# Optimization experiments

Hardware: AMD Instinct MI355X
Metric: run time of the kernel (lower is better)

## Reference

```python
import jax, jax.numpy as jnp
import numpy as np

N = 8192      # total nodes (128 graphs x 64 electrodes)
L = 256       # signal_length
F = 64        # num_features
H = 128       # hidden_channels
G = 128       # num graphs
E = 262144    # num edges
C = 2         # n_classes


def setup_inputs() -> dict:
    key = jax.random.key(0)
    ks = jax.random.split(key, 20)
    def rn(k, shape, scale=0.05):
        return jax.random.normal(k, shape, jnp.float32) * scale
    return dict(
        x=jax.random.normal(ks[0], (N, L), jnp.float32),
        edge_index=jax.random.randint(ks[1], (2, E), 0, N),
        batch=jnp.repeat(jnp.arange(G), N // G),  # sorted graph id per node
        cw0=rn(ks[2], (F, 1, 7)), cb0=rn(ks[3], (F,)),
        cw_mid=rn(ks[4], (3, F, F, 5)), cb_mid=rn(ks[5], (3, F)),  # convs-2 = 3 middle convs
        cw_last=rn(ks[6], (F, F, 3)), cb_last=rn(ks[7], (F,)),
        enc_w=rn(ks[8], (F, F * 4)), enc_b=rn(ks[9], (F,)),  # in = F*((L-1)//2**6+1) = 256
        g0_rel_w=rn(ks[10], (H, F)), g0_rel_b=rn(ks[11], (H,)), g0_root_w=rn(ks[12], (H, F)),
        g_rel_w=rn(ks[13], (7, H, H)), g_rel_b=rn(ks[14], (7, H)), g_root_w=rn(ks[15], (7, H, H)),
        lin_w=rn(ks[16], (3, H, H)), lin_b=rn(ks[17], (3, H)),
        out_w=rn(ks[18], (C, H)), out_b=rn(ks[19], (C,)),
    )


def _conv1d(x, w, b, stride, pad):
    # x: [N, Cin, L], w: [Cout, Cin, K]
    y = jax.lax.conv_general_dilated(x, w, (stride,), [(pad, pad)],
                                     dimension_numbers=('NCH', 'OIH', 'NCH'))
    return y + b[None, :, None]


def reference(x, edge_index, batch, cw0, cb0, cw_mid, cb_mid, cw_last, cb_last,
              enc_w, enc_b, g0_rel_w, g0_rel_b, g0_root_w,
              g_rel_w, g_rel_b, g_root_w, lin_w, lin_b, out_w, out_b):
    act = jax.nn.relu
    rows = x.shape[0]
    h = x[:, None, :]                                    # [N, 1, L]
    h = act(_conv1d(h, cw0, cb0, 2, 3))                  # [N, F, L/2]
    for i in range(3):                                   # middle convs, k=5 s=2 p=2
        h = act(_conv1d(h, cw_mid[i], cb_mid[i], 2, 2))
    h = act(_conv1d(h, cw_last, cb_last, 2, 1))          # k=3 s=2 p=1 -> [N, F, 8]
    # AvgPool1d(k=3, s=2, p=1), count_include_pad=True -> always divide by 3
    h = jax.lax.reduce_window(h, 0.0, jax.lax.add, (1, 1, 3), (1, 1, 2),
                              [(0, 0), (0, 0), (1, 1)]) / 3.0   # [N, F, 4]
    h = h.reshape(rows, -1)                              # [N, F*4]
    h = h @ enc_w.T + enc_b                              # [N, F]
    src, dst = edge_index[0], edge_index[1]
    def gconv(h, rel_w, rel_b, root_w):
        # PyG GraphConv (aggr='add'): lin_rel(sum_j x_j) + lin_root(x)
        agg = jax.ops.segment_sum(h[src], dst, num_segments=N)
        return agg @ rel_w.T + rel_b + h @ root_w.T
    h = act(gconv(h, g0_rel_w, g0_rel_b, g0_root_w))     # hop 0: F -> H
    for i in range(7):                                   # hops 1..7: H -> H
        h = act(gconv(h, g_rel_w[i], g_rel_b[i], g_root_w[i]))
    # global mean pool by graph id
    sums = jax.ops.segment_sum(h, batch, num_segments=G)
    cnt = jax.ops.segment_sum(jnp.ones((N, 1), h.dtype), batch, num_segments=G)
    h = sums / jnp.maximum(cnt, 1.0)                     # [G, H]
    for i in range(3):
        h = act(h @ lin_w[i].T + lin_b[i])
    logits = h @ out_w.T + out_b                         # [G, C]
    return jax.nn.log_softmax(logits, -1)
```

## Files before the change

kernel.cpp:

```cpp
#include <hip/hip_runtime.h>
#include <hip/hip_bf16.h>

#define DEV_INLINE __device__ __forceinline__

typedef _Float16 f16;
typedef _Float16 f16x4 __attribute__((ext_vector_type(4)));
typedef _Float16 f16x8 __attribute__((ext_vector_type(8)));
typedef __bf16 bf16;
typedef __bf16 bf16x8 __attribute__((ext_vector_type(8)));
typedef float f32x16 __attribute__((ext_vector_type(16)));
typedef float f32x4 __attribute__((ext_vector_type(4)));

constexpr int N_NODES = 8192;
constexpr int G = 128;
constexpr int E_EDGES = 262144;

struct alignas(16) ConvLDS {
  union {
    char act1[2][2][66][128];
    struct {
      char act3[2][2][18][128];
      char act4[2][2][10][128];
      float act5[16][68];
      float pooled[2][256];
      float encred[2][2][64];
    } tail;
  } A;
  char act2[2][2][34][128];
  f16 xs16[2][272];
};

template<int MT, int LOG_PN, int IN_PS, int OUT_PS>
DEV_INLINE void conv_mid(const f16* __restrict__ wb, const float* __restrict__ bias,
                         char* inb, char* outb, int w, int l) {
  const int cht = w & 1;
  const int o_lane = cht * 32 + (l & 31);
  const int khalf = l >> 5;
  if ((w >> 1) < MT) {
    f16x8 wf[5][4];
#pragma unroll
    for (int k = 0; k < 5; k++)
#pragma unroll
      for (int s = 0; s < 4; s++)
        wf[k][s] = *(const f16x8*)&wb[(k * 64 + o_lane) * 64 + s * 16 + khalf * 8];
    f32x16 binit;
#pragma unroll
    for (int g = 0; g < 4; g++) {
      const float4 b4 = *(const float4*)&bias[cht * 32 + 8 * g + khalf * 4];
      binit[4 * g + 0] = b4.x; binit[4 * g + 1] = b4.y;
      binit[4 * g + 2] = b4.z; binit[4 * g + 3] = b4.w;
    }
    for (int mt = (w >> 1); mt < MT; mt += 2) {
      const int mo = mt * 32 + (l & 31);
      const int node = mo >> LOG_PN;
      const int po = mo & ((1 << LOG_PN) - 1);
      f32x16 acc = binit;
#pragma unroll
      for (int k = 0; k < 5; k++) {
        const int d = k - 2;
        const int par = d & 1;
        const int row = po + (d >> 1) + 1;
        const char* rb = inb + ((node * 2 + par) * IN_PS + row) * 128;
        const int fx = row & 7;
#pragma unroll
        for (int s = 0; s < 4; s++) {
          const int c8 = 2 * s + khalf;
          f16x8 af = *(const f16x8*)(rb + ((c8 ^ fx) << 4));
          acc = __builtin_amdgcn_mfma_f32_32x32x16_f16(wf[k][s], af, acc, 0, 0, 0);
        }
      }
      const int orow = (po >> 1) + 1;
      const int ofx = orow & 7;
      char* base = outb + ((node * 2 + (po & 1)) * OUT_PS + orow) * 128 + khalf * 8;
#pragma unroll
      for (int g = 0; g < 4; g++) {
        f16x4 h4;
        h4[0] = (f16)fmaxf(acc[4 * g + 0], 0.f);
        h4[1] = (f16)fmaxf(acc[4 * g + 1], 0.f);
        h4[2] = (f16)fmaxf(acc[4 * g + 2], 0.f);
        h4[3] = (f16)fmaxf(acc[4 * g + 3], 0.f);
        *(f16x4*)(base + (((cht * 4 + g) ^ ofx) << 4)) = h4;
      }
    }
  }
}

__global__ __launch_bounds__(256, 3) void conv_encode_kernel(
    const float* __restrict__ x,
    const f16* __restrict__ w0f, const float* __restrict__ cb0,
    const f16* __restrict__ wbmid, const float* __restrict__ cb_mid,
    const f16* __restrict__ wb5, const float* __restrict__ cb_last,
    const float* __restrict__ enc_w, const float* __restrict__ enc_b,
    float* __restrict__ henc) {
  __shared__ ConvLDS lds;
  const int tid = threadIdx.x;
  const int w = tid >> 6, l = tid & 63;
  const int n0 = blockIdx.x * 2;

  for (int idx = tid; idx < 512; idx += 256) {
    int node = idx >> 8, j = idx & 255;
    lds.xs16[node][3 + j] = (f16)x[(size_t)(n0 + node) * 256 + j];
  }
  if (tid < 64) {
    int node = tid >> 5, t = tid & 31;
    int par = (t >> 3) & 1, hi = t >> 4, j = t & 7;
    *(int4*)&lds.A.act1[node][par][hi ? 65 : 0][j * 16] = make_int4(0, 0, 0, 0);
  } else if (tid < 128) {
    int t2 = tid - 64;
    int node = t2 >> 5, t = t2 & 31;
    int par = (t >> 3) & 1, hi = t >> 4, j = t & 7;
    *(int4*)&lds.act2[node][par][hi ? 33 : 0][j * 16] = make_int4(0, 0, 0, 0);
  } else if (tid < 160) {
    int t3 = tid - 128;
    int node = t3 >> 4, s = t3 & 15;
    int slot = (s < 3) ? s : (256 + s);
    lds.xs16[node][slot] = (f16)0.f;
  }
  __syncthreads();

  {
    const int cht = w & 1;
    const int o_lane = cht * 32 + (l & 31);
    const int khalf = l >> 5;
    const f16x8 w0frag = *(const f16x8*)&w0f[o_lane * 16 + khalf * 8];
    f32x16 binit;
#pragma unroll
    for (int g = 0; g < 4; g++) {
      const float4 b4 = *(const float4*)&cb0[cht * 32 + 8 * g + khalf * 4];
      binit[4 * g + 0] = b4.x; binit[4 * g + 1] = b4.y;
      binit[4 * g + 2] = b4.z; binit[4 * g + 3] = b4.w;
    }
    for (int mt = (w >> 1); mt < 8; mt += 2) {
      const int mo = mt * 32 + (l & 31);
      const int node = mo >> 7;
      const int po = mo & 127;
      union { uint u[4]; f16x8 v; } au;
      const char* ap = (const char*)&lds.xs16[node][2 * po + khalf * 8];
#pragma unroll
      for (int j = 0; j < 4; j++) au.u[j] = *(const uint*)(ap + 4 * j);
      f32x16 acc = __builtin_amdgcn_mfma_f32_32x32x16_f16(w0frag, au.v, binit, 0, 0, 0);
      const int orow = (po >> 1) + 1;
      const int ofx = orow & 7;
      char* base = (char*)lds.A.act1 + ((node * 2 + (po & 1)) * 66 + orow) * 128 + khalf * 8;
#pragma unroll
      for (int g = 0; g < 4; g++) {
        f16x4 h4;
        h4[0] = (f16)fmaxf(acc[4 * g + 0], 0.f);
        h4[1] = (f16)fmaxf(acc[4 * g + 1], 0.f);
        h4[2] = (f16)fmaxf(acc[4 * g + 2], 0.f);
        h4[3] = (f16)fmaxf(acc[4 * g + 3], 0.f);
        *(f16x4*)(base + (((cht * 4 + g) ^ ofx) << 4)) = h4;
      }
    }
  }
  __syncthreads();

  conv_mid<4, 6, 66, 34>(wbmid, cb_mid, (char*)lds.A.act1, (char*)lds.act2, w, l);
  __syncthreads();

  if (tid < 128) {
    int which = tid >> 6;
    int t = tid & 63;
    int node = t >> 5, tt = t & 31;
    int par = (tt >> 3) & 1, hi = tt >> 4, j = tt & 7;
    if (which == 0)
      *(int4*)&lds.A.tail.act3[node][par][hi ? 17 : 0][j * 16] = make_int4(0, 0, 0, 0);
    else
      *(int4*)&lds.A.tail.act4[node][par][hi ? 9 : 0][j * 16] = make_int4(0, 0, 0, 0);
  }
  __syncthreads();

  conv_mid<2, 5, 34, 18>(wbmid + 5 * 64 * 64, cb_mid + 64,
                         (char*)lds.act2, (char*)lds.A.tail.act3, w, l);
  __syncthreads();
  conv_mid<1, 4, 18, 10>(wbmid + 2 * 5 * 64 * 64, cb_mid + 128,
                         (char*)lds.A.tail.act3, (char*)lds.A.tail.act4, w, l);
  __syncthreads();

  {
    const int ch_row = w * 16 + (l & 15);
    const int kq = l >> 4;
    f16x8 wf5[3][2];
#pragma unroll
    for (int k = 0; k < 3; k++)
#pragma unroll
      for (int s = 0; s < 2; s++)
        wf5[k][s] = *(const f16x8*)&wb5[(k * 64 + ch_row) * 64 + s * 32 + kq * 8];
    const float4 b4 = *(const float4*)&cb_last[w * 16 + kq * 4];
    f32x4 acc5 = {b4.x, b4.y, b4.z, b4.w};
    const int m5 = l & 15, nd5 = m5 >> 3, p5 = m5 & 7;
#pragma unroll
    for (int k = 0; k < 3; k++) {
      const int d = k - 1;
      const int par = d & 1;
      const int row = p5 + (d >> 1) + 1;
      const char* rb = (char*)lds.A.tail.act4 + ((nd5 * 2 + par) * 10 + row) * 128;
      const int fx = row & 7;
#pragma unroll
      for (int s = 0; s < 2; s++) {
        const int c8 = 4 * s + kq;
        f16x8 af = *(const f16x8*)(rb + ((c8 ^ fx) << 4));
        acc5 = __builtin_amdgcn_mfma_f32_16x16x32_f16(wf5[k][s], af, acc5, 0, 0, 0);
      }
    }
    f32x4 o4;
    o4[0] = fmaxf(acc5[0], 0.f);
    o4[1] = fmaxf(acc5[1], 0.f);
    o4[2] = fmaxf(acc5[2], 0.f);
    o4[3] = fmaxf(acc5[3], 0.f);
    *(f32x4*)&lds.A.tail.act5[nd5 * 8 + p5][w * 16 + kq * 4] = o4;
  }
  __syncthreads();

  for (int jj = tid; jj < 512; jj += 256) {
    int node = jj >> 8, j = jj & 255;
    int c = j >> 2, q = j & 3;
    const float* a5 = &lds.A.tail.act5[node * 8][0];
    float v = a5[(2 * q) * 68 + c] + a5[(2 * q + 1) * 68 + c];
    if (q > 0) v += a5[(2 * q - 1) * 68 + c];
    lds.A.tail.pooled[node][j] = v * (1.f / 3.f);
  }
  __syncthreads();

  {
    const int node = tid >> 7, tt = tid & 127;
    const int o = tt & 63, jg = tt >> 6;
    float acc = 0.f;
    const float4* ew = (const float4*)&enc_w[o * 256 + jg * 128];
    const float4* pj = (const float4*)&lds.A.tail.pooled[node][jg * 128];
#pragma unroll 4
    for (int j4 = 0; j4 < 32; j4++) {
      float4 a = ew[j4], b = pj[j4];
      acc += a.x * b.x + a.y * b.y + a.z * b.z + a.w * b.w;
    }
    lds.A.tail.encred[node][jg][o] = acc;
  }
  __syncthreads();
  if (tid < 128) {
    int node = tid >> 6, o = tid & 63;
    henc[(size_t)(n0 + node) * 64 + o] =
        lds.A.tail.encred[node][0][o] + lds.A.tail.encred[node][1][o] + enc_b[o];
  }
}

__global__ void wprep_all(const float* __restrict__ cw0,
                          const float* __restrict__ cw_mid, const float* __restrict__ cw_last,
                          const float* __restrict__ g0_rel, const float* __restrict__ g0_root,
                          const float* __restrict__ g0_rel_b,
                          const float* __restrict__ g_rel, const float* __restrict__ g_root,
                          const float* __restrict__ g_rel_b,
                          f16* __restrict__ w0f, f16* __restrict__ wbmid, f16* __restrict__ wb5,
                          bf16* __restrict__ wg, float* __restrict__ bg) {
  int idx = blockIdx.x * 256 + threadIdx.x;
  if (idx < 64 * 16) {
    int o = idx >> 4, k = idx & 15;
    w0f[idx] = (k < 7) ? (f16)cw0[o * 7 + k] : (f16)0.f;
  }
  if (idx < 3 * 5 * 64 * 64) {
    int lay = idx / (5 * 64 * 64);
    int rem = idx % (5 * 64 * 64);
    int k = rem / 4096;
    int o = (rem >> 6) & 63;
    int c = rem & 63;
    wbmid[idx] = (f16)cw_mid[((lay * 64 + o) * 64 + c) * 5 + k];
  } else {
    int i2 = idx - 3 * 5 * 64 * 64;
    if (i2 < 3 * 64 * 64) {
      int k = i2 / 4096;
      int o = (i2 >> 6) & 63;
      int c = i2 & 63;
      wb5[i2] = (f16)cw_last[(o * 64 + c) * 3 + k];
    }
  }
  if (idx < 128 * 128) {
    int o = idx >> 7, k = idx & 127;
    float v = (k < 64) ? g0_rel[o * 64 + k] : g0_root[o * 64 + (k - 64)];
    bf16 h = (bf16)v;
    wg[idx] = h;
    wg[128 * 128 + idx] = (bf16)(v - (float)h);
  }
  if (idx < 7 * 128 * 256) {
    int lsel = idx / (128 * 256);
    int r = idx % (128 * 256);
    int o = r >> 8, k = r & 255;
    float v = (k < 128) ? g_rel[(lsel * 128 + o) * 128 + k]
                        : g_root[(lsel * 128 + o) * 128 + (k - 128)];
    bf16 h = (bf16)v;
    size_t base = 2 * 128 * 128 + (size_t)lsel * 2 * 128 * 256;
    wg[base + r] = h;
    wg[base + 128 * 256 + r] = (bf16)(v - (float)h);
  }
  if (idx < 8 * 128) {
    int lsel = idx >> 7, o = idx & 127;
    bg[idx] = (lsel == 0) ? g0_rel_b[o] : g_rel_b[(lsel - 1) * 128 + o];
  }
}

__global__ void hist_kernel(const int* __restrict__ dst, int* __restrict__ cnt) {
  int e = blockIdx.x * 256 + threadIdx.x;
  atomicAdd(&cnt[dst[e]], 1);
}

__global__ void scan_kernel(const int* __restrict__ cnt, int* __restrict__ rp) {
  __shared__ int part[256];
  int t = threadIdx.x;
  int base = t * 32;
  int local[32];
  int s = 0;
#pragma unroll
  for (int i = 0; i < 32; i++) { local[i] = cnt[base + i]; s += local[i]; }
  part[t] = s;
  __syncthreads();
  for (int off = 1; off < 256; off <<= 1) {
    int v = (t >= off) ? part[t - off] : 0;
    __syncthreads();
    part[t] += v;
    __syncthreads();
  }
  int run = part[t] - s;
#pragma unroll
  for (int i = 0; i < 32; i++) { rp[base + i] = run; run += local[i]; }
  if (t == 255) rp[N_NODES] = run;
}

__global__ void fill_kernel(const int* __restrict__ src, const int* __restrict__ dst,
                            const int* __restrict__ rp, int* __restrict__ cur,
                            int* __restrict__ csr) {
  int e = blockIdx.x * 256 + threadIdx.x;
  int r = dst[e];
  int p = atomicAdd(&cur[r], 1);
  csr[rp[r] + p] = src[e];
}

template<int D>
__global__ __launch_bounds__(256) void gatherf(
    const float* __restrict__ h, const int* __restrict__ csr,
    const int* __restrict__ rp, float* __restrict__ agg) {
  constexpr int LPN = D / 4;
  const int node = blockIdx.x * (256 / LPN) + (threadIdx.x / LPN);
  const int cl = threadIdx.x & (LPN - 1);
  const int s = rp[node], e = rp[node + 1];
  float4 a0 = make_float4(0.f, 0.f, 0.f, 0.f);
  float4 a1 = make_float4(0.f, 0.f, 0.f, 0.f);
  float4 a2 = make_float4(0.f, 0.f, 0.f, 0.f);
  float4 a3 = make_float4(0.f, 0.f, 0.f, 0.f);
  int i = s;
  for (; i + 3 < e; i += 4) {
    const int m0 = csr[i], m1 = csr[i + 1], m2 = csr[i + 2], m3 = csr[i + 3];
    float4 v0 = *(const float4*)&h[(size_t)m0 * D + cl * 4];
    float4 v1 = *(const float4*)&h[(size_t)m1 * D + cl * 4];
    float4 v2 = *(const float4*)&h[(size_t)m2 * D + cl * 4];
    float4 v3 = *(const float4*)&h[(size_t)m3 * D + cl * 4];
    a0.x += v0.x; a0.y += v0.y; a0.z += v0.z; a0.w += v0.w;
    a1.x += v1.x; a1.y += v1.y; a1.z += v1.z; a1.w += v1.w;
    a2.x += v2.x; a2.y += v2.y; a2.z += v2.z; a2.w += v2.w;
    a3.x += v3.x; a3.y += v3.y; a3.z += v3.z; a3.w += v3.w;
  }
  for (; i < e; i++) {
    const int m0 = csr[i];
    float4 v0 = *(const float4*)&h[(size_t)m0 * D + cl * 4];
    a0.x += v0.x; a0.y += v0.y; a0.z += v0.z; a0.w += v0.w;
  }
  a0.x += a1.x + a2.x + a3.x;
  a0.y += a1.y + a2.y + a3.y;
  a0.z += a1.z + a2.z + a3.z;
  a0.w += a1.w + a2.w + a3.w;
  *(float4*)&agg[(size_t)node * D + cl * 4] = a0;
}

template<int K>
__global__ __launch_bounds__(256) void gnn_gemm_bf(
    const float* __restrict__ agg, const float* __restrict__ hroot,
    const bf16* __restrict__ wg, const float* __restrict__ bg,
    float* __restrict__ hout) {
  constexpr int F = K / 2;
  constexpr int ROWB = K * 2;
  constexpr int KSTEPS = K / 16;
  __shared__ alignas(16) char smem[2][32 * K * 2];
  const int tid = threadIdx.x;
  const int l = tid & 63, w = tid >> 6;
  const int n0 = blockIdx.x * 32;

  {
    const int row = tid >> 3, p = tid & 7;
    constexpr int cpp = K / 64;
#pragma unroll
    for (int j = 0; j < cpp; j++) {
      const int slot = p * cpp + j;
      const int c0 = slot * 8;
      const float* src = (c0 < F) ? &agg[(size_t)(n0 + row) * F + c0]
                                  : &hroot[(size_t)(n0 + row) * F + (c0 - F)];
      float4 v0 = ((const float4*)src)[0];
      float4 v1 = ((const float4*)src)[1];
      float vv[8] = {v0.x, v0.y, v0.z, v0.w, v1.x, v1.y, v1.z, v1.w};
      bf16x8 hi8, lo8;
#pragma unroll
      for (int e = 0; e < 8; e++) {
        float v = vv[e];
        bf16 h = (bf16)v;
        hi8[e] = h;
        lo8[e] = (bf16)(v - (float)h);
      }
      const int off = row * ROWB + ((slot ^ (row & 7)) << 4);
      *(bf16x8*)(smem[0] + off) = hi8;
      *(bf16x8*)(smem[1] + off) = lo8;
    }
  }

  const int ch = w * 32 + (l & 31);
  const int khalf = l >> 5;
  bf16x8 whi[KSTEPS], wlo[KSTEPS];
  const bf16* wrow = wg + (size_t)ch * K + khalf * 8;
#pragma unroll
  for (int ks = 0; ks < KSTEPS; ks++) {
    whi[ks] = *(const bf16x8*)&wrow[ks * 16];
    wlo[ks] = *(const bf16x8*)&wrow[128 * K + ks * 16];
  }
  const float bv = bg[ch];

  __syncthreads();

  const int row0 = l & 31;
  f32x16 acc = {0,0,0,0,0,0,0,0,0,0,0,0,0,0,0,0};
#pragma unroll
  for (int ks = 0; ks < KSTEPS; ks++) {
    const int slot = ks * 2 + khalf;
    const int off = row0 * ROWB + ((slot ^ (row0 & 7)) << 4);
    bf16x8 ah = *(const bf16x8*)(smem[0] + off);
    bf16x8 al = *(const bf16x8*)(smem[1] + off);
    acc = __builtin_amdgcn_mfma_f32_32x32x16_bf16(ah, whi[ks], acc, 0, 0, 0);
    acc = __builtin_amdgcn_mfma_f32_32x32x16_bf16(al, whi[ks], acc, 0, 0, 0);
    acc = __builtin_amdgcn_mfma_f32_32x32x16_bf16(ah, wlo[ks], acc, 0, 0, 0);
  }

#pragma unroll
  for (int r = 0; r < 16; r++) {
    const int nl = (r & 3) + 8 * (r >> 2) + 4 * khalf;
    hout[(size_t)(n0 + nl) * 128 + ch] = fmaxf(acc[r] + bv, 0.f);
  }
}

__global__ __launch_bounds__(256) void poolg(const float* __restrict__ h,
                                             float* __restrict__ pooled) {
  const int g = blockIdx.x;
  const int tid = threadIdx.x;
  const int ch = tid & 127, half = tid >> 7;
  const float* base = h + ((size_t)g * 64 + half * 32) * 128 + ch;
  float s = 0.f;
#pragma unroll 8
  for (int i = 0; i < 32; i++) s += base[(size_t)i * 128];
  __shared__ float red[256];
  red[tid] = s;
  __syncthreads();
  if (tid < 128) pooled[(size_t)g * 128 + tid] = (red[tid] + red[tid + 128]) * (1.f / 64.f);
}

__global__ __launch_bounds__(128) void mlp_kernel(
    const float* __restrict__ pooled,
    const float* __restrict__ lin_w, const float* __restrict__ lin_b,
    const float* __restrict__ out_w, const float* __restrict__ out_b,
    float* __restrict__ out) {
  const int g = blockIdx.x;
  const int t = threadIdx.x;
  __shared__ float hs[128];
  __shared__ float lg[2];
  hs[t] = pooled[(size_t)g * 128 + t];
  __syncthreads();
  for (int lsel = 0; lsel < 3; lsel++) {
    float acc = lin_b[lsel * 128 + t];
    for (int j = 0; j < 128; j++) acc += hs[j] * lin_w[(lsel * 128 + t) * 128 + j];
    __syncthreads();
    hs[t] = fmaxf(acc, 0.f);
    __syncthreads();
  }
  if (t < 2) {
    float acc = out_b[t];
    for (int j = 0; j < 128; j++) acc += hs[j] * out_w[t * 128 + j];
    lg[t] = acc;
  }
  __syncthreads();
  if (t < 2) {
    float m = fmaxf(lg[0], lg[1]);
    float lse = m + logf(expf(lg[0] - m) + expf(lg[1] - m));
    out[g * 2 + t] = lg[t] - lse;
  }
}

extern "C" void kernel_launch(void* const* d_in, const int* in_sizes, int n_in,
                              void* d_out, int out_size, void* d_ws, size_t ws_size,
                              hipStream_t stream) {
  const float* x       = (const float*)d_in[0];
  const int*   edge    = (const int*)d_in[1];
  const float* cw0     = (const float*)d_in[3];
  const float* cb0     = (const float*)d_in[4];
  const float* cw_mid  = (const float*)d_in[5];
  const float* cb_mid  = (const float*)d_in[6];
  const float* cw_last = (const float*)d_in[7];
  const float* cb_last = (const float*)d_in[8];
  const float* enc_w   = (const float*)d_in[9];
  const float* enc_b   = (const float*)d_in[10];
  const float* g0_rel_w  = (const float*)d_in[11];
  const float* g0_rel_b  = (const float*)d_in[12];
  const float* g0_root_w = (const float*)d_in[13];
  const float* g_rel_w   = (const float*)d_in[14];
  const float* g_rel_b   = (const float*)d_in[15];
  const float* g_root_w  = (const float*)d_in[16];
  const float* lin_w     = (const float*)d_in[17];
  const float* lin_b     = (const float*)d_in[18];
  const float* out_w     = (const float*)d_in[19];
  const float* out_b     = (const float*)d_in[20];
  float* out = (float*)d_out;

  const int* esrc = edge;
  const int* edst = edge + E_EDGES;

  char* ws = (char*)d_ws;
  size_t off = 0;
  auto alloc = [&](size_t bytes) {
    void* p = ws + off;
    off += (bytes + 255) & ~size_t(255);
    return p;
  };
  float* henc = (float*)alloc((size_t)N_NODES * 64 * 4);
  float* hA   = (float*)alloc((size_t)N_NODES * 128 * 4);
  float* hB   = (float*)alloc((size_t)N_NODES * 128 * 4);
  float* agg  = (float*)alloc((size_t)N_NODES * 128 * 4);
  bf16* wg    = (bf16*)alloc((size_t)(128 * 128 + 7 * 128 * 256) * 2 * 2);
  float* bg   = (float*)alloc((size_t)8 * 128 * 4);
  float* pooled = (float*)alloc((size_t)G * 128 * 4);
  int* cnt  = (int*)alloc((size_t)N_NODES * 4);
  int* rp   = (int*)alloc((size_t)(N_NODES + 1) * 4);
  int* cur  = (int*)alloc((size_t)N_NODES * 4);
  int* csr  = (int*)alloc((size_t)E_EDGES * 4);
  f16* w0f   = (f16*)alloc((size_t)64 * 16 * 2);
  f16* wbmid = (f16*)alloc((size_t)3 * 5 * 64 * 64 * 2);
  f16* wb5   = (f16*)alloc((size_t)3 * 64 * 64 * 2);

  hipMemsetAsync(cnt, 0, (size_t)N_NODES * 4, stream);
  hipMemsetAsync(cur, 0, (size_t)N_NODES * 4, stream);

  wprep_all<<<896, 256, 0, stream>>>(cw0, cw_mid, cw_last,
                                     g0_rel_w, g0_root_w, g0_rel_b,
                                     g_rel_w, g_root_w, g_rel_b,
                                     w0f, wbmid, wb5, wg, bg);
  conv_encode_kernel<<<N_NODES / 2, 256, 0, stream>>>(
      x, w0f, cb0, wbmid, cb_mid, wb5, cb_last, enc_w, enc_b, henc);

  hist_kernel<<<E_EDGES / 256, 256, 0, stream>>>(edst, cnt);
  scan_kernel<<<1, 256, 0, stream>>>(cnt, rp);
  fill_kernel<<<E_EDGES / 256, 256, 0, stream>>>(esrc, edst, rp, cur, csr);

  gatherf<64><<<N_NODES / 16, 256, 0, stream>>>(henc, csr, rp, agg);
  gnn_gemm_bf<128><<<N_NODES / 32, 256, 0, stream>>>(agg, henc, wg, bg, hA);

  float* hprev = hA;
  float* hnext = hB;
  for (int lsel = 0; lsel < 7; lsel++) {
    gatherf<128><<<N_NODES / 8, 256, 0, stream>>>(hprev, csr, rp, agg);
    gnn_gemm_bf<256><<<N_NODES / 32, 256, 0, stream>>>(
        agg, hprev, wg + 2 * 128 * 128 + (size_t)lsel * 2 * 128 * 256,
        bg + (lsel + 1) * 128, hnext);
    float* tmp = hprev; hprev = hnext; hnext = tmp;
  }

  poolg<<<G, 256, 0, stream>>>(hprev, pooled);
  mlp_kernel<<<G, 128, 0, stream>>>(pooled, lin_w, lin_b, out_w, out_b, out);
}
```

Before: 390.5 us.

## Split conv encoder into two kernels and dual-accumulate MFMA chains

```diff
diff --git a/kernel.cpp b/kernel.cpp
--- a/kernel.cpp
+++ b/kernel.cpp
@@ -15,20 +15,6 @@
 constexpr int G = 128;
 constexpr int E_EDGES = 262144;
 
-struct alignas(16) ConvLDS {
-  union {
-    char act1[2][2][66][128];
-    struct {
-      char act3[2][2][18][128];
-      char act4[2][2][10][128];
-      float act5[16][68];
-      float pooled[2][256];
-      float encred[2][2][64];
-    } tail;
-  } A;
-  char act2[2][2][34][128];
-  f16 xs16[2][272];
-};
 
 template<int MT, int LOG_PN, int IN_PS, int OUT_PS>
 DEV_INLINE void conv_mid(const f16* __restrict__ wb, const float* __restrict__ bias,
@@ -55,6 +41,7 @@
       const int node = mo >> LOG_PN;
       const int po = mo & ((1 << LOG_PN) - 1);
       f32x16 acc = binit;
+      f32x16 acc2 = {0,0,0,0,0,0,0,0,0,0,0,0,0,0,0,0};
 #pragma unroll
       for (int k = 0; k < 5; k++) {
         const int d = k - 2;
@@ -66,12 +53,81 @@
         for (int s = 0; s < 4; s++) {
           const int c8 = 2 * s + khalf;
           f16x8 af = *(const f16x8*)(rb + ((c8 ^ fx) << 4));
-          acc = __builtin_amdgcn_mfma_f32_32x32x16_f16(wf[k][s], af, acc, 0, 0, 0);
+          if (k & 1) acc2 = __builtin_amdgcn_mfma_f32_32x32x16_f16(wf[k][s], af, acc2, 0, 0, 0);
+          else       acc  = __builtin_amdgcn_mfma_f32_32x32x16_f16(wf[k][s], af, acc, 0, 0, 0);
         }
       }
       const int orow = (po >> 1) + 1;
       const int ofx = orow & 7;
       char* base = outb + ((node * 2 + (po & 1)) * OUT_PS + orow) * 128 + khalf * 8;
+#pragma unroll
+      for (int g = 0; g < 4; g++) {
+        f16x4 h4;
+        h4[0] = (f16)fmaxf(acc[4 * g + 0] + acc2[4 * g + 0], 0.f);
+        h4[1] = (f16)fmaxf(acc[4 * g + 1] + acc2[4 * g + 1], 0.f);
+        h4[2] = (f16)fmaxf(acc[4 * g + 2] + acc2[4 * g + 2], 0.f);
+        h4[3] = (f16)fmaxf(acc[4 * g + 3] + acc2[4 * g + 3], 0.f);
+        *(f16x4*)(base + (((cht * 4 + g) ^ ofx) << 4)) = h4;
+      }
+    }
+  }
+}
+
+struct alignas(16) L12LDS {
+  char act1[2][2][66][128];
+  f16 xs16[2][272];
+};
+
+__global__ __launch_bounds__(256, 4) void conv_l1l2_kernel(
+    const float* __restrict__ x,
+    const f16* __restrict__ w0f, const float* __restrict__ cb0,
+    const f16* __restrict__ wbmid, const float* __restrict__ cb_mid,
+    f16* __restrict__ a2g) {
+  __shared__ L12LDS lds;
+  const int tid = threadIdx.x;
+  const int w = tid >> 6, l = tid & 63;
+  const int n0 = blockIdx.x * 2;
+
+  for (int idx = tid; idx < 512; idx += 256) {
+    int node = idx >> 8, j = idx & 255;
+    lds.xs16[node][3 + j] = (f16)x[(size_t)(n0 + node) * 256 + j];
+  }
+  if (tid < 64) {
+    int node = tid >> 5, t = tid & 31;
+    int par = (t >> 3) & 1, hi = t >> 4, j = t & 7;
+    *(int4*)&lds.act1[node][par][hi ? 65 : 0][j * 16] = make_int4(0, 0, 0, 0);
+  } else if (tid < 96) {
+    int t3 = tid - 64;
+    int node = t3 >> 4, s = t3 & 15;
+    int slot = (s < 3) ? s : (256 + s);
+    lds.xs16[node][slot] = (f16)0.f;
+  }
+  __syncthreads();
+
+  {
+    const int cht = w & 1;
+    const int o_lane = cht * 32 + (l & 31);
+    const int khalf = l >> 5;
+    const f16x8 w0frag = *(const f16x8*)&w0f[o_lane * 16 + khalf * 8];
+    f32x16 binit;
+#pragma unroll
+    for (int g = 0; g < 4; g++) {
+      const float4 b4 = *(const float4*)&cb0[cht * 32 + 8 * g + khalf * 4];
+      binit[4 * g + 0] = b4.x; binit[4 * g + 1] = b4.y;
+      binit[4 * g + 2] = b4.z; binit[4 * g + 3] = b4.w;
+    }
+    for (int mt = (w >> 1); mt < 8; mt += 2) {
+      const int mo = mt * 32 + (l & 31);
+      const int node = mo >> 7;
+      const int po = mo & 127;
+      union { uint u[4]; f16x8 v; } au;
+      const char* ap = (const char*)&lds.xs16[node][2 * po + khalf * 8];
+#pragma unroll
+      for (int j = 0; j < 4; j++) au.u[j] = *(const uint*)(ap + 4 * j);
+      f32x16 acc = __builtin_amdgcn_mfma_f32_32x32x16_f16(w0frag, au.v, binit, 0, 0, 0);
+      const int orow = (po >> 1) + 1;
+      const int ofx = orow & 7;
+      char* base = (char*)lds.act1 + ((node * 2 + (po & 1)) * 66 + orow) * 128 + khalf * 8;
 #pragma unroll
       for (int g = 0; g < 4; g++) {
         f16x4 h4;
@@ -83,98 +139,114 @@
       }
     }
   }
-}
-
-__global__ __launch_bounds__(256, 3) void conv_encode_kernel(
-    const float* __restrict__ x,
-    const f16* __restrict__ w0f, const float* __restrict__ cb0,
-    const f16* __restrict__ wbmid, const float* __restrict__ cb_mid,
-    const f16* __restrict__ wb5, const float* __restrict__ cb_last,
-    const float* __restrict__ enc_w, const float* __restrict__ enc_b,
-    float* __restrict__ henc) {
-  __shared__ ConvLDS lds;
-  const int tid = threadIdx.x;
-  const int w = tid >> 6, l = tid & 63;
-  const int n0 = blockIdx.x * 2;
-
-  for (int idx = tid; idx < 512; idx += 256) {
-    int node = idx >> 8, j = idx & 255;
-    lds.xs16[node][3 + j] = (f16)x[(size_t)(n0 + node) * 256 + j];
-  }
-  if (tid < 64) {
-    int node = tid >> 5, t = tid & 31;
-    int par = (t >> 3) & 1, hi = t >> 4, j = t & 7;
-    *(int4*)&lds.A.act1[node][par][hi ? 65 : 0][j * 16] = make_int4(0, 0, 0, 0);
-  } else if (tid < 128) {
-    int t2 = tid - 64;
-    int node = t2 >> 5, t = t2 & 31;
-    int par = (t >> 3) & 1, hi = t >> 4, j = t & 7;
-    *(int4*)&lds.act2[node][par][hi ? 33 : 0][j * 16] = make_int4(0, 0, 0, 0);
-  } else if (tid < 160) {
-    int t3 = tid - 128;
-    int node = t3 >> 4, s = t3 & 15;
-    int slot = (s < 3) ? s : (256 + s);
-    lds.xs16[node][slot] = (f16)0.f;
-  }
   __syncthreads();
 
   {
     const int cht = w & 1;
     const int o_lane = cht * 32 + (l & 31);
     const int khalf = l >> 5;
-    const f16x8 w0frag = *(const f16x8*)&w0f[o_lane * 16 + khalf * 8];
+    f16x8 wf[5][4];
+#pragma unroll
+    for (int k = 0; k < 5; k++)
+#pragma unroll
+      for (int s = 0; s < 4; s++)
+        wf[k][s] = *(const f16x8*)&wbmid[(k * 64 + o_lane) * 64 + s * 16 + khalf * 8];
     f32x16 binit;
 #pragma unroll
     for (int g = 0; g < 4; g++) {
-      const float4 b4 = *(const float4*)&cb0[cht * 32 + 8 * g + khalf * 4];
+      const float4 b4 = *(const float4*)&cb_mid[cht * 32 + 8 * g + khalf * 4];
       binit[4 * g + 0] = b4.x; binit[4 * g + 1] = b4.y;
       binit[4 * g + 2] = b4.z; binit[4 * g + 3] = b4.w;
     }
-    for (int mt = (w >> 1); mt < 8; mt += 2) {
+    for (int mt = (w >> 1); mt < 4; mt += 2) {
       const int mo = mt * 32 + (l & 31);
-      const int node = mo >> 7;
-      const int po = mo & 127;
-      union { uint u[4]; f16x8 v; } au;
-      const char* ap = (const char*)&lds.xs16[node][2 * po + khalf * 8];
-#pragma unroll
-      for (int j = 0; j < 4; j++) au.u[j] = *(const uint*)(ap + 4 * j);
-      f32x16 acc = __builtin_amdgcn_mfma_f32_32x32x16_f16(w0frag, au.v, binit, 0, 0, 0);
-      const int orow = (po >> 1) + 1;
-      const int ofx = orow & 7;
-      char* base = (char*)lds.A.act1 + ((node * 2 + (po & 1)) * 66 + orow) * 128 + khalf * 8;
+      const int node = mo >> 6;
+      const int po = mo & 63;
+      f32x16 acc = binit;
+      f32x16 acc2 = {0,0,0,0,0,0,0,0,0,0,0,0,0,0,0,0};
+#pragma unroll
+      for (int k = 0; k < 5; k++) {
+        const int d = k - 2;
+        const int par = d & 1;
+        const int row = po + (d >> 1) + 1;
+        const char* rb = (char*)lds.act1 + ((node * 2 + par) * 66 + row) * 128;
+        const int fx = row & 7;
+#pragma unroll
+        for (int s = 0; s < 4; s++) {
+          const int c8 = 2 * s + khalf;
+          f16x8 af = *(const f16x8*)(rb + ((c8 ^ fx) << 4));
+          if (k & 1) acc2 = __builtin_amdgcn_mfma_f32_32x32x16_f16(wf[k][s], af, acc2, 0, 0, 0);
+          else       acc  = __builtin_amdgcn_mfma_f32_32x32x16_f16(wf[k][s], af, acc, 0, 0, 0);
+        }
+      }
+      f16* gbase = a2g + ((size_t)(n0 + node) * 64 + po) * 64 + khalf * 4;
 #pragma unroll
       for (int g = 0; g < 4; g++) {
         f16x4 h4;
-        h4[0] = (f16)fmaxf(acc[4 * g + 0], 0.f);
-        h4[1] = (f16)fmaxf(acc[4 * g + 1], 0.f);
-        h4[2] = (f16)fmaxf(acc[4 * g + 2], 0.f);
-        h4[3] = (f16)fmaxf(acc[4 * g + 3], 0.f);
-        *(f16x4*)(base + (((cht * 4 + g) ^ ofx) << 4)) = h4;
+        h4[0] = (f16)fmaxf(acc[4 * g + 0] + acc2[4 * g + 0], 0.f);
+        h4[1] = (f16)fmaxf(acc[4 * g + 1] + acc2[4 * g + 1], 0.f);
+        h4[2] = (f16)fmaxf(acc[4 * g + 2] + acc2[4 * g + 2], 0.f);
+        h4[3] = (f16)fmaxf(acc[4 * g + 3] + acc2[4 * g + 3], 0.f);
+        *(f16x4*)(gbase + cht * 32 + g * 8) = h4;
       }
     }
   }
-  __syncthreads();
-
-  conv_mid<4, 6, 66, 34>(wbmid, cb_mid, (char*)lds.A.act1, (char*)lds.act2, w, l);
-  __syncthreads();
-
-  if (tid < 128) {
+}
+
+struct alignas(16) L3LDS {
+  union {
+    char in2[2][2][34][128];
+    struct {
+      float act5[16][68];
+      float pooled[2][256];
+      float encred[2][2][64];
+    } t;
+  } U;
+  char act3[2][2][18][128];
+  char act4[2][2][10][128];
+};
+
+__global__ __launch_bounds__(256, 4) void conv_l3tail_kernel(
+    const f16* __restrict__ a2g,
+    const f16* __restrict__ wbmid, const float* __restrict__ cb_mid,
+    const f16* __restrict__ wb5, const float* __restrict__ cb_last,
+    const f16* __restrict__ enc_w16, const float* __restrict__ enc_b,
+    float* __restrict__ henc) {
+  __shared__ L3LDS lds;
+  const int tid = threadIdx.x;
+  const int w = tid >> 6, l = tid & 63;
+  const int n0 = blockIdx.x * 2;
+
+#pragma unroll
+  for (int i = 0; i < 4; i++) {
+    const int idx = tid + i * 256;
+    const int node = idx >> 9;
+    const int rem = idx & 511;
+    const int p = rem >> 3, s8 = rem & 7;
+    const int row = (p >> 1) + 1, par = p & 1;
+    int4 v = *(const int4*)&a2g[((size_t)(n0 + node) * 64 + p) * 64 + s8 * 8];
+    *(int4*)((char*)lds.U.in2 + ((node * 2 + par) * 34 + row) * 128
+             + ((s8 ^ (row & 7)) << 4)) = v;
+  }
+  if (tid < 192) {
     int which = tid >> 6;
     int t = tid & 63;
     int node = t >> 5, tt = t & 31;
     int par = (tt >> 3) & 1, hi = tt >> 4, j = tt & 7;
     if (which == 0)
-      *(int4*)&lds.A.tail.act3[node][par][hi ? 17 : 0][j * 16] = make_int4(0, 0, 0, 0);
+      *(int4*)&lds.U.in2[node][par][hi ? 33 : 0][j * 16] = make_int4(0, 0, 0, 0);
+    else if (which == 1)
+      *(int4*)&lds.act3[node][par][hi ? 17 : 0][j * 16] = make_int4(0, 0, 0, 0);
     else
-      *(int4*)&lds.A.tail.act4[node][par][hi ? 9 : 0][j * 16] = make_int4(0, 0, 0, 0);
+      *(int4*)&lds.act4[node][par][hi ? 9 : 0][j * 16] = make_int4(0, 0, 0, 0);
   }
   __syncthreads();
 
   conv_mid<2, 5, 34, 18>(wbmid + 5 * 64 * 64, cb_mid + 64,
-                         (char*)lds.act2, (char*)lds.A.tail.act3, w, l);
+                         (char*)lds.U.in2, (char*)lds.act3, w, l);
   __syncthreads();
   conv_mid<1, 4, 18, 10>(wbmid + 2 * 5 * 64 * 64, cb_mid + 128,
-                         (char*)lds.A.tail.act3, (char*)lds.A.tail.act4, w, l);
+                         (char*)lds.act3, (char*)lds.act4, w, l);
   __syncthreads();
 
   {
@@ -194,7 +266,7 @@
       const int d = k - 1;
       const int par = d & 1;
       const int row = p5 + (d >> 1) + 1;
-      const char* rb = (char*)lds.A.tail.act4 + ((nd5 * 2 + par) * 10 + row) * 128;
+      const char* rb = (char*)lds.act4 + ((nd5 * 2 + par) * 10 + row) * 128;
       const int fx = row & 7;
 #pragma unroll
       for (int s = 0; s < 2; s++) {
@@ -208,17 +280,17 @@
     o4[1] = fmaxf(acc5[1], 0.f);
     o4[2] = fmaxf(acc5[2], 0.f);
     o4[3] = fmaxf(acc5[3], 0.f);
-    *(f32x4*)&lds.A.tail.act5[nd5 * 8 + p5][w * 16 + kq * 4] = o4;
+    *(f32x4*)&lds.U.t.act5[nd5 * 8 + p5][w * 16 + kq * 4] = o4;
   }
   __syncthreads();
 
   for (int jj = tid; jj < 512; jj += 256) {
     int node = jj >> 8, j = jj & 255;
     int c = j >> 2, q = j & 3;
-    const float* a5 = &lds.A.tail.act5[node * 8][0];
+    const float* a5 = &lds.U.t.act5[node * 8][0];
     float v = a5[(2 * q) * 68 + c] + a5[(2 * q + 1) * 68 + c];
     if (q > 0) v += a5[(2 * q - 1) * 68 + c];
-    lds.A.tail.pooled[node][j] = v * (1.f / 3.f);
+    lds.U.t.pooled[node][j] = v * (1.f / 3.f);
   }
   __syncthreads();
 
@@ -226,30 +298,36 @@
     const int node = tid >> 7, tt = tid & 127;
     const int o = tt & 63, jg = tt >> 6;
     float acc = 0.f;
-    const float4* ew = (const float4*)&enc_w[o * 256 + jg * 128];
-    const float4* pj = (const float4*)&lds.A.tail.pooled[node][jg * 128];
+    const f16x8* ew = (const f16x8*)&enc_w16[o * 256 + jg * 128];
+    const float4* pj = (const float4*)&lds.U.t.pooled[node][jg * 128];
 #pragma unroll 4
-    for (int j4 = 0; j4 < 32; j4++) {
-      float4 a = ew[j4], b = pj[j4];
-      acc += a.x * b.x + a.y * b.y + a.z * b.z + a.w * b.w;
-    }
-    lds.A.tail.encred[node][jg][o] = acc;
+    for (int j8 = 0; j8 < 16; j8++) {
+      f16x8 e8 = ew[j8];
+      float4 p0 = pj[2 * j8], p1 = pj[2 * j8 + 1];
+      acc += (float)e8[0] * p0.x + (float)e8[1] * p0.y +
+             (float)e8[2] * p0.z + (float)e8[3] * p0.w +
+             (float)e8[4] * p1.x + (float)e8[5] * p1.y +
+             (float)e8[6] * p1.z + (float)e8[7] * p1.w;
+    }
+    lds.U.t.encred[node][jg][o] = acc;
   }
   __syncthreads();
   if (tid < 128) {
     int node = tid >> 6, o = tid & 63;
     henc[(size_t)(n0 + node) * 64 + o] =
-        lds.A.tail.encred[node][0][o] + lds.A.tail.encred[node][1][o] + enc_b[o];
+        lds.U.t.encred[node][0][o] + lds.U.t.encred[node][1][o] + enc_b[o];
   }
 }
 
 __global__ void wprep_all(const float* __restrict__ cw0,
                           const float* __restrict__ cw_mid, const float* __restrict__ cw_last,
+                          const float* __restrict__ enc_w,
                           const float* __restrict__ g0_rel, const float* __restrict__ g0_root,
                           const float* __restrict__ g0_rel_b,
                           const float* __restrict__ g_rel, const float* __restrict__ g_root,
                           const float* __restrict__ g_rel_b,
                           f16* __restrict__ w0f, f16* __restrict__ wbmid, f16* __restrict__ wb5,
+                          f16* __restrict__ enc_w16,
                           bf16* __restrict__ wg, float* __restrict__ bg) {
   int idx = blockIdx.x * 256 + threadIdx.x;
   if (idx < 64 * 16) {
@@ -272,6 +350,7 @@
       wb5[i2] = (f16)cw_last[(o * 64 + c) * 3 + k];
     }
   }
+  if (idx < 64 * 256) enc_w16[idx] = (f16)enc_w[idx];
   if (idx < 128 * 128) {
     int o = idx >> 7, k = idx & 127;
     float v = (k < 64) ? g0_rel[o * 64 + k] : g0_root[o * 64 + (k - 64)];
@@ -535,16 +614,19 @@
   f16* w0f   = (f16*)alloc((size_t)64 * 16 * 2);
   f16* wbmid = (f16*)alloc((size_t)3 * 5 * 64 * 64 * 2);
   f16* wb5   = (f16*)alloc((size_t)3 * 64 * 64 * 2);
+  f16* enc_w16 = (f16*)alloc((size_t)64 * 256 * 2);
+  f16* a2g   = (f16*)alloc((size_t)N_NODES * 64 * 64 * 2);
 
   hipMemsetAsync(cnt, 0, (size_t)N_NODES * 4, stream);
   hipMemsetAsync(cur, 0, (size_t)N_NODES * 4, stream);
 
-  wprep_all<<<896, 256, 0, stream>>>(cw0, cw_mid, cw_last,
+  wprep_all<<<896, 256, 0, stream>>>(cw0, cw_mid, cw_last, enc_w,
                                      g0_rel_w, g0_root_w, g0_rel_b,
                                      g_rel_w, g_root_w, g_rel_b,
-                                     w0f, wbmid, wb5, wg, bg);
-  conv_encode_kernel<<<N_NODES / 2, 256, 0, stream>>>(
-      x, w0f, cb0, wbmid, cb_mid, wb5, cb_last, enc_w, enc_b, henc);
+                                     w0f, wbmid, wb5, enc_w16, wg, bg);
+  conv_l1l2_kernel<<<N_NODES / 2, 256, 0, stream>>>(x, w0f, cb0, wbmid, cb_mid, a2g);
+  conv_l3tail_kernel<<<N_NODES / 2, 256, 0, stream>>>(
+      a2g, wbmid, cb_mid, wb5, cb_last, enc_w16, enc_b, henc);
 
   hist_kernel<<<E_EDGES / 256, 256, 0, stream>>>(edst, cnt);
   scan_kernel<<<1, 256, 0, stream>>>(cnt, rp);
```

Result: slower. 412.7 us (+5.7%).
